# Kernel optimization log

Hardware: AMD Instinct MI355X
Metric: run time of the kernel (lower is better)

The kernel has to match this reference:

```python
import jax, jax.numpy as jnp
import numpy as np

B_CHUNK = 5          # hardcoded self.B in the module
GAMMA = 0.9865
BATCH, SEQ, FEAT, DIM = 8, 4000, 256, 256


def setup_inputs() -> dict:
    key = jax.random.key(0)
    ks = jax.random.split(key, 6)
    xq = jax.random.normal(ks[0], (BATCH, SEQ, FEAT), jnp.float32)
    xk = jax.random.normal(ks[1], (BATCH, SEQ, FEAT), jnp.float32)
    xv = jax.random.normal(ks[2], (BATCH, SEQ, FEAT), jnp.float32)
    scale = 1.0 / np.sqrt(FEAT).astype(np.float32)
    Wq = jax.random.normal(ks[3], (FEAT, DIM), jnp.float32) * scale
    Wk = jax.random.normal(ks[4], (FEAT, DIM), jnp.float32) * scale
    Wv = jax.random.normal(ks[5], (FEAT, DIM), jnp.float32) * scale
    return {"xq": xq, "xk": xk, "xv": xv, "Wq": Wq, "Wk": Wk, "Wv": Wv}


def reference(xq, xk, xv, Wq, Wk, Wv):
    gamma = jnp.float32(GAMMA)
    B = B_CHUNK
    b, seq, _ = xq.shape
    dim = Wq.shape[1]
    n = seq // B  # number of chunks

    # projections, chunked: [b, n, B, dim]
    Q = (xq @ Wq).reshape(b, n, B, dim)
    K = (xk @ Wk).reshape(b, n, B, dim)
    V = (xv @ Wv).reshape(b, n, B, dim)

    chunk_idx = jnp.arange(n, dtype=jnp.float32)
    # Z[i] = gamma^(B - i - 1) (per-chunk scalar, as in original)
    Z = gamma ** (jnp.float32(B) - chunk_idx - 1.0)
    Vz = V * Z[None, :, None, None]

    # intra-chunk decay matrix: L[i,j] = gamma^(j-i) for i >= j, else 0
    pos = jnp.arange(B, dtype=jnp.float32)
    L = jnp.tril(gamma ** (pos[None, :] - pos[:, None]))

    # intra-chunk term: (Q K^T * L) @ V, vectorized over all chunks
    S = jnp.einsum('bnid,bnjd->bnij', Q, K)          # [b, n, B, B]
    intra = jnp.einsum('bnij,bnjd->bnid', S * L, V)  # [b, n, B, dim]

    # cross-chunk recurrence: R[i] = K_i^T Vz_i + gamma^B R[i-1]
    # X[i-1] += Q_i @ R[i-1] * gamma^(i+1)
    Qn = jnp.moveaxis(Q, 1, 0)   # [n, b, B, dim]
    Kn = jnp.moveaxis(K, 1, 0)
    Vzn = jnp.moveaxis(Vz, 1, 0)
    gB = gamma ** B

    def step(R_prev, inp):
        qi, ki, vzi, i = inp
        cross_prev = jnp.einsum('bod,bde->boe', qi, R_prev) * gamma ** (i + 1.0)
        R_new = jnp.einsum('bod,boe->bde', ki, vzi) + gB * R_prev
        return R_new, cross_prev

    R0 = jnp.zeros((b, dim, dim), xq.dtype)
    _, ys = jax.lax.scan(step, R0, (Qn, Kn, Vzn, chunk_idx))  # ys[i] = cross for chunk i-1
    cross = jnp.concatenate([ys[1:], jnp.zeros_like(ys[:1])], axis=0)  # last chunk has no cross term
    cross = jnp.moveaxis(cross, 0, 1)  # [b, n, B, dim]

    X = intra + cross
    return X.reshape(b, seq, dim)
```

## Files before the change

### kernel.cpp

```cpp
#include <hip/hip_runtime.h>
#include <cmath>

#define GAMMA 0.9865f
#define L2G   -0.01960905f
#define BATCH 8
#define SEQ   4000
#define CSUP  25
#define GSUP  32
#define RPG   125

typedef _Float16 half8 __attribute__((ext_vector_type(8)));
typedef _Float16 half4 __attribute__((ext_vector_type(4)));
typedef float    floatx4 __attribute__((ext_vector_type(4)));

__device__ __forceinline__ float gpow(float e) { return exp2f(e * L2G); }

__global__ __launch_bounds__(256) void wt_convert(
    const float* __restrict__ Wq, const float* __restrict__ Wk, const float* __restrict__ Wv,
    _Float16* __restrict__ Wt) {
    int t = blockIdx.x * 256 + threadIdx.x;
    int mat = t >> 16, rem = t & 65535;
    int n = rem >> 8, k = rem & 255;
    const float* W = (mat == 0) ? Wq : (mat == 1) ? Wk : Wv;
    Wt[(size_t)mat * 65536 + n * 256 + k] = (_Float16)W[k * 256 + n];
}

__global__ __launch_bounds__(256, 2) void qkv_gemm_f16(
    const float* __restrict__ xq, const float* __restrict__ xk, const float* __restrict__ xv,
    const _Float16* __restrict__ WtAll,
    _Float16* __restrict__ Qb, _Float16* __restrict__ Kb, _Float16* __restrict__ Vb) {
    int op = blockIdx.y;
    const float* x = (op == 0) ? xq : (op == 1) ? xk : xv;
    const _Float16* Wt = WtAll + (size_t)op * 65536;
    _Float16* dst = (op == 0) ? Qb : (op == 1) ? Kb : Vb;

    __shared__ _Float16 Xs[128][40];
    __shared__ _Float16 WsT[256][40];

    int t = threadIdx.x;
    int lane = t & 63, wave = t >> 6;
    int ln = lane & 15, q8 = (lane >> 4) << 3, q4 = (lane >> 4) << 2;
    int row0 = blockIdx.x * 128;

    floatx4 acc[8][4] = {};

    for (int dt = 0; dt < 8; ++dt) {
        int k0 = dt * 32;
#pragma unroll
        for (int i = 0; i < 4; ++i) {
            int idx = t + i * 256;
            int m = idx >> 3, kk = (idx & 7) << 2;
            floatx4 v = *(const floatx4*)&x[(size_t)(row0 + m) * 256 + k0 + kk];
            half4 h; h[0] = (_Float16)v[0]; h[1] = (_Float16)v[1];
            h[2] = (_Float16)v[2]; h[3] = (_Float16)v[3];
            *(half4*)&Xs[m][kk] = h;
        }
#pragma unroll
        for (int i = 0; i < 4; ++i) {
            int idx = t + i * 256;
            int n = idx >> 2, kk = (idx & 3) << 3;
            *(half8*)&WsT[n][kk] = *(const half8*)&Wt[n * 256 + k0 + kk];
        }
        __syncthreads();
        half8 af[8];
#pragma unroll
        for (int mi = 0; mi < 8; ++mi) af[mi] = *(const half8*)&Xs[mi * 16 + ln][q8];
#pragma unroll
        for (int ni = 0; ni < 4; ++ni) {
            half8 bf = *(const half8*)&WsT[(wave * 4 + ni) * 16 + ln][q8];
#pragma unroll
            for (int mi = 0; mi < 8; ++mi)
                acc[mi][ni] = __builtin_amdgcn_mfma_f32_16x16x32_f16(af[mi], bf, acc[mi][ni], 0, 0, 0);
        }
        __syncthreads();
    }
#pragma unroll
    for (int mi = 0; mi < 8; ++mi)
#pragma unroll
        for (int ni = 0; ni < 4; ++ni)
#pragma unroll
            for (int r = 0; r < 4; ++r) {
                int row = row0 + mi * 16 + q4 + r;
                int col = (wave * 4 + ni) * 16 + ln;
                dst[(size_t)row * 256 + col] = (_Float16)acc[mi][ni][r];
            }
}

__global__ __launch_bounds__(256, 2) void chunk_states_mfma(
    const _Float16* __restrict__ Kb, const _Float16* __restrict__ Vb,
    _Float16* __restrict__ Wh) {
    int eh = blockIdx.x, g = blockIdx.y, b = blockIdx.z;
    int t = threadIdx.x, lane = t & 63, wave = t >> 6;
    int ln = lane & 15, q8 = (lane >> 4) << 3, q4 = (lane >> 4) << 2;
    __shared__ _Float16 Vs[32 * 137];
    __shared__ _Float16 Ks[32 * 265];
    size_t base_row = (size_t)b * SEQ + g * RPG;
    floatx4 acc[8][4] = {};
    for (int kt = 0; kt < 4; ++kt) {
        int r0 = kt * 32;
#pragma unroll
        for (int i = 0; i < 2; ++i) {
            int idx = t + i * 256;
            int r = idx >> 4, e8 = (idx & 15) << 3;
            half8 v = {};
            if (r0 + r < RPG) {
                v = *(const half8*)&Vb[(base_row + r0 + r) * 256 + eh * 128 + e8];
                int mloc = (r0 + r) / 5;
                float a = gpow((float)(149 - 6 * mloc));
#pragma unroll
                for (int z = 0; z < 8; ++z) v[z] = (_Float16)((float)v[z] * a);
            }
#pragma unroll
            for (int z = 0; z < 8; ++z) Vs[r * 137 + e8 + z] = v[z];
        }
#pragma unroll
        for (int i = 0; i < 4; ++i) {
            int idx = t + i * 256;
            int r = idx >> 5, d8 = (idx & 31) << 3;
            half8 v = {};
            if (r0 + r < RPG) v = *(const half8*)&Kb[(base_row + r0 + r) * 256 + d8];
#pragma unroll
            for (int z = 0; z < 8; ++z) Ks[r * 265 + d8 + z] = v[z];
        }
        __syncthreads();
        half8 Af[8], Bf[4];
#pragma unroll
        for (int mi = 0; mi < 8; ++mi)
#pragma unroll
            for (int j = 0; j < 8; ++j) Af[mi][j] = Vs[(q8 + j) * 137 + mi * 16 + ln];
#pragma unroll
        for (int ni = 0; ni < 4; ++ni)
#pragma unroll
            for (int j = 0; j < 8; ++j) Bf[ni][j] = Ks[(q8 + j) * 265 + wave * 64 + ni * 16 + ln];
#pragma unroll
        for (int mi = 0; mi < 8; ++mi)
#pragma unroll
            for (int ni = 0; ni < 4; ++ni)
                acc[mi][ni] = __builtin_amdgcn_mfma_f32_16x16x32_f16(Af[mi], Bf[ni], acc[mi][ni], 0, 0, 0);
        __syncthreads();
    }
    size_t ob = ((size_t)(g * 8 + b)) << 16;
#pragma unroll
    for (int mi = 0; mi < 8; ++mi)
#pragma unroll
        for (int ni = 0; ni < 4; ++ni)
#pragma unroll
            for (int r = 0; r < 4; ++r) {
                int e = eh * 128 + mi * 16 + q4 + r;
                int d = wave * 64 + ni * 16 + ln;
                Wh[ob + (size_t)e * 256 + d] = (_Float16)acc[mi][ni][r];
            }
}

__global__ __launch_bounds__(256) void state_scan(
    const _Float16* __restrict__ Wh, _Float16* __restrict__ SprevT) {
    int t = blockIdx.x * 256 + threadIdx.x;
    int b = t >> 14;
    int idx = (t & 16383) << 2;
    const float gF = gpow(150.0f);
    float s[4] = {};
    for (int g = 0; g < GSUP; ++g) {
        size_t o = (((size_t)(g * 8 + b)) << 16) + idx;
        half4 w = *(const half4*)&Wh[o];
        half4 sv;
#pragma unroll
        for (int z = 0; z < 4; ++z) { sv[z] = (_Float16)s[z]; s[z] = (float)w[z] + gF * s[z]; }
        *(half4*)&SprevT[o] = sv;
    }
}

__global__ __launch_bounds__(256) void intra_sc(
    const _Float16* __restrict__ Qb, const _Float16* __restrict__ Kb, float* __restrict__ scw) {
    int b = blockIdx.y;
    int j = blockIdx.x * 4 + (threadIdx.x >> 6);
    int lane = threadIdx.x & 63;
    size_t base = ((size_t)b * SEQ + j * 5) * 256 + lane * 4;
    half4 qv[5], kv[5];
#pragma unroll
    for (int p = 0; p < 5; ++p) {
        qv[p] = *(const half4*)&Qb[base + p * 256];
        kv[p] = *(const half4*)&Kb[base + p * 256];
    }
#pragma unroll
    for (int p = 0; p < 5; ++p)
#pragma unroll
        for (int q = 0; q <= p; ++q) {
            float s = 0.f;
#pragma unroll
            for (int z = 0; z < 4; ++z) s += (float)qv[p][z] * (float)kv[q][z];
#pragma unroll
            for (int off = 32; off; off >>= 1) s += __shfl_xor(s, off, 64);
            if (lane == 0) scw[((size_t)b * 800 + j) * 25 + p * 5 + q] = s * gpow((float)(q - p));
        }
}

__global__ __launch_bounds__(256, 3) void cross_f16(
    const _Float16* __restrict__ Qb, const _Float16* __restrict__ Kb,
    const _Float16* __restrict__ Vb, const _Float16* __restrict__ SprevT,
    const float* __restrict__ scw, float* __restrict__ out) {
    int eq = blockIdx.x, g = blockIdx.y, b = blockIdx.z;
    int e0 = eq * 64;
    int t = threadIdx.x;
    int lane = t & 63, wave = t >> 6;
    int ln = lane & 15, q8 = (lane >> 4) << 3, q4 = (lane >> 4) << 2;
    int m4 = (wave >> 1) * 4;
    int c4 = (wave & 1) * 4;
    int e2 = (wave & 1) * 2;

    __shared__ float rtab[25];
    __shared__ float gtabm[25];
    __shared__ _Float16 PsB[128 * 130];
    __shared__ _Float16 VsB[64 * 130];

    if (t < 25) { rtab[t] = gpow((float)(6 * t + 7)); gtabm[t] = gpow((float)(6 * (t + 1))); }

    size_t kvbase = (size_t)b * SEQ + g * RPG;
    size_t sb = ((size_t)(g * 8 + b)) << 16;
    size_t qrow0 = (size_t)b * SEQ;

#pragma unroll
    for (int i = 0; i < 4; ++i) {
        int idx = t + i * 256;
        int cp = idx >> 3, e8 = (idx & 7) << 3;
        half8 v = {};
        if (cp < 125) v = *(const half8*)&Vb[(kvbase + cp) * 256 + e0 + e8];
#pragma unroll
        for (int z = 0; z < 8; ++z) VsB[(e8 + z) * 130 + cp] = v[z];
    }

    floatx4 pacc[4][4] = {};
    floatx4 acc[4][2] = {};

    for (int dt = 0; dt < 8; ++dt) {
        int d0 = dt * 32;
        half8 af[4];
#pragma unroll
        for (int mi = 0; mi < 4; ++mi) {
            int rp = (m4 + mi) * 16 + ln;
            int qr = g * RPG + 5 + rp;
            half8 v = {};
            if (rp < 125 && qr < SEQ) v = *(const half8*)&Qb[(qrow0 + qr) * 256 + d0 + q8];
            af[mi] = v;
        }
#pragma unroll
        for (int ci = 0; ci < 4; ++ci) {
            int cp = (c4 + ci) * 16 + ln;
            half8 bf = {};
            if (cp < 125) bf = *(const half8*)&Kb[(kvbase + cp) * 256 + d0 + q8];
#pragma unroll
            for (int mi = 0; mi < 4; ++mi)
                pacc[mi][ci] = __builtin_amdgcn_mfma_f32_16x16x32_f16(af[mi], bf, pacc[mi][ci], 0, 0, 0);
        }
#pragma unroll
        for (int ei = 0; ei < 2; ++ei) {
            half8 bf = *(const half8*)&SprevT[sb + (size_t)(e0 + (e2 + ei) * 16 + ln) * 256 + d0 + q8];
#pragma unroll
            for (int mi = 0; mi < 4; ++mi)
                acc[mi][ei] = __builtin_amdgcn_mfma_f32_16x16x32_f16(af[mi], bf, acc[mi][ei], 0, 0, 0);
        }
    }

    __syncthreads();

#pragma unroll
    for (int mi = 0; mi < 4; ++mi)
#pragma unroll
        for (int r = 0; r < 4; ++r) {
            int rp = (m4 + mi) * 16 + q4 + r;
            int rc = rp / 5;
            float rs = 0.f;
            if (rp < 125 && !(g == GSUP - 1 && rc == CSUP - 1)) rs = rtab[rc];
            acc[mi][0][r] *= rs;
            acc[mi][1][r] *= rs;
        }

#pragma unroll
    for (int mi = 0; mi < 4; ++mi)
#pragma unroll
        for (int ci = 0; ci < 4; ++ci)
#pragma unroll
            for (int r = 0; r < 4; ++r) {
                int rp = (m4 + mi) * 16 + q4 + r;
                int cp = (c4 + ci) * 16 + ln;
                int rc = rp / 5, cc = cp / 5;
                float w = 0.f;
                if (rp < 125 && cp < 125 && cc <= rc && !(g == GSUP - 1 && rc == CSUP - 1))
                    w = gtabm[rc - cc];
                PsB[rp * 130 + cp] = (_Float16)(pacc[mi][ci][r] * w);
            }
    __syncthreads();

#pragma unroll
    for (int ct = 0; ct < 4; ++ct) {
        int cp0 = ct * 32;
        half8 paf[4];
#pragma unroll
        for (int mi = 0; mi < 4; ++mi)
#pragma unroll
            for (int j = 0; j < 8; ++j)
                paf[mi][j] = PsB[((m4 + mi) * 16 + ln) * 130 + cp0 + q8 + j];
#pragma unroll
        for (int ei = 0; ei < 2; ++ei) {
            half8 bv;
#pragma unroll
            for (int j = 0; j < 8; ++j)
                bv[j] = VsB[((e2 + ei) * 16 + ln) * 130 + cp0 + q8 + j];
#pragma unroll
            for (int mi = 0; mi < 4; ++mi)
                acc[mi][ei] = __builtin_amdgcn_mfma_f32_16x16x32_f16(paf[mi], bv, acc[mi][ei], 0, 0, 0);
        }
    }

#pragma unroll
    for (int mi = 0; mi < 4; ++mi)
#pragma unroll
        for (int r = 0; r < 4; ++r) {
            int rp = (m4 + mi) * 16 + q4 + r;
            if (rp < 125) {
                int rc = rp / 5, pp = rp - rc * 5;
                const float* srow = scw + ((size_t)b * 800 + g * 25 + rc) * 25 + pp * 5;
                float a0 = acc[mi][0][r], a1 = acc[mi][1][r];
                for (int q = 0; q <= pp; ++q) {
                    float s = srow[q];
                    a0 += s * (float)VsB[(e2 * 16 + ln) * 130 + rc * 5 + q];
                    a1 += s * (float)VsB[((e2 + 1) * 16 + ln) * 130 + rc * 5 + q];
                }
                size_t orow = ((size_t)b * SEQ + g * RPG + rp) * 256;
                out[orow + e0 + e2 * 16 + ln] = a0;
                out[orow + e0 + (e2 + 1) * 16 + ln] = a1;
            }
        }
}

extern "C" void kernel_launch(void* const* d_in, const int* in_sizes, int n_in,
                              void* d_out, int out_size, void* d_ws, size_t ws_size,
                              hipStream_t stream) {
    const float* xq = (const float*)d_in[0];
    const float* xk = (const float*)d_in[1];
    const float* xv = (const float*)d_in[2];
    const float* Wq = (const float*)d_in[3];
    const float* Wk = (const float*)d_in[4];
    const float* Wv = (const float*)d_in[5];
    float* out = (float*)d_out;

    const size_t NELEM = (size_t)SEQ * BATCH * 256;
    _Float16* Qb = (_Float16*)d_ws;
    _Float16* Kb = Qb + NELEM;
    _Float16* Vb = Kb + NELEM;
    _Float16* Wt = Vb + NELEM;
    _Float16* Wh = Wt + 196608;
    _Float16* SprevT = Wh + (size_t)GSUP * BATCH * 65536;
    float* scw = (float*)(SprevT + (size_t)GSUP * BATCH * 65536);

    wt_convert<<<dim3(768), 256, 0, stream>>>(Wq, Wk, Wv, Wt);
    qkv_gemm_f16<<<dim3(250, 3), 256, 0, stream>>>(xq, xk, xv, Wt, Qb, Kb, Vb);
    chunk_states_mfma<<<dim3(2, 32, 8), 256, 0, stream>>>(Kb, Vb, Wh);
    state_scan<<<dim3(512), 256, 0, stream>>>(Wh, SprevT);
    intra_sc<<<dim3(200, 8), 256, 0, stream>>>(Qb, Kb, scw);
    cross_f16<<<dim3(4, 32, 8), 256, 0, stream>>>(Qb, Kb, Vb, SprevT, scw, out);
}
```

Baseline: 290.5 us.

## Retile cross kernel by row halves with LDS-staged double-buffered Q/K and tiled state

The cross kernel now tiles over two 64-row halves with all 256 output columns per block, instead of four 64-column slabs. This removes the redundant recomputation of the QK^T score block across column slabs. Q and K tiles are staged through double-buffered LDS with prefetch. The state-scan writes the prefix states in an MFMA-fragment-tiled layout so the B operands load contiguously, and V is transposed into LDS in two halves that reuse the staging memory. The trade-off is half as many blocks (less parallelism), higher accumulator register pressure, and more LDS per block.

```diff
diff --git a/kernel.cpp b/kernel.cpp
--- a/kernel.cpp
+++ b/kernel.cpp
@@ -153,19 +153,23 @@
 }
 
 __global__ __launch_bounds__(256) void state_scan(
-    const _Float16* __restrict__ Wh, _Float16* __restrict__ SprevT) {
+    const _Float16* __restrict__ Wh, _Float16* __restrict__ Sx) {
     int t = blockIdx.x * 256 + threadIdx.x;
     int b = t >> 14;
-    int idx = (t & 16383) << 2;
+    int r = t & 16383;
+    int e = r >> 6;
+    int dc = (r & 63) << 2;
+    int T = (dc >> 5) * 16 + (e >> 4);
+    int off = T * 512 + (e & 15) * 32 + (dc & 31);
     const float gF = gpow(150.0f);
     float s[4] = {};
     for (int g = 0; g < GSUP; ++g) {
-        size_t o = (((size_t)(g * 8 + b)) << 16) + idx;
-        half4 w = *(const half4*)&Wh[o];
+        size_t ibase = ((size_t)(g * 8 + b)) << 16;
+        half4 w = *(const half4*)&Wh[ibase + e * 256 + dc];
         half4 sv;
 #pragma unroll
         for (int z = 0; z < 4; ++z) { sv[z] = (_Float16)s[z]; s[z] = (float)w[z] + gF * s[z]; }
-        *(half4*)&SprevT[o] = sv;
+        *(half4*)&Sx[ibase + off] = sv;
     }
 }
 
@@ -196,140 +200,168 @@
 
 __global__ __launch_bounds__(256, 3) void cross_f16(
     const _Float16* __restrict__ Qb, const _Float16* __restrict__ Kb,
-    const _Float16* __restrict__ Vb, const _Float16* __restrict__ SprevT,
+    const _Float16* __restrict__ Vb, const _Float16* __restrict__ Sx,
     const float* __restrict__ scw, float* __restrict__ out) {
-    int eq = blockIdx.x, g = blockIdx.y, b = blockIdx.z;
-    int e0 = eq * 64;
+    int rh = blockIdx.x, g = blockIdx.y, b = blockIdx.z;
     int t = threadIdx.x;
-    int lane = t & 63, wave = t >> 6;
-    int ln = lane & 15, q8 = (lane >> 4) << 3, q4 = (lane >> 4) << 2;
-    int m4 = (wave >> 1) * 4;
-    int c4 = (wave & 1) * 4;
-    int e2 = (wave & 1) * 2;
-
-    __shared__ float rtab[25];
-    __shared__ float gtabm[25];
-    __shared__ _Float16 PsB[128 * 130];
-    __shared__ _Float16 VsB[64 * 130];
+    int lane = t & 63, eq = t >> 6;
+    int ln = lane & 15, qd = lane >> 4;
+    int q8 = qd << 3, q4 = qd << 2;
+
+    __shared__ __align__(16) char smem[52432];
+    _Float16* stage = (_Float16*)smem;
+    _Float16* PsB = (_Float16*)(smem + 34816);
+    float* rtab = (float*)(smem + 52224);
+    float* gtabm = rtab + 25;
 
     if (t < 25) { rtab[t] = gpow((float)(6 * t + 7)); gtabm[t] = gpow((float)(6 * (t + 1))); }
 
     size_t kvbase = (size_t)b * SEQ + g * RPG;
-    size_t sb = ((size_t)(g * 8 + b)) << 16;
-    size_t qrow0 = (size_t)b * SEQ;
-
-#pragma unroll
-    for (int i = 0; i < 4; ++i) {
-        int idx = t + i * 256;
-        int cp = idx >> 3, e8 = (idx & 7) << 3;
-        half8 v = {};
-        if (cp < 125) v = *(const half8*)&Vb[(kvbase + cp) * 256 + e0 + e8];
-#pragma unroll
-        for (int z = 0; z < 8; ++z) VsB[(e8 + z) * 130 + cp] = v[z];
-    }
-
-    floatx4 pacc[4][4] = {};
-    floatx4 acc[4][2] = {};
-
+    size_t sxb = ((size_t)(g * 8 + b)) << 16;
+    size_t qtop = (size_t)b * SEQ;
+
+    int sm = t >> 2;
+    int skk = (t & 3) << 3;
+    int rpgQ = rh * 64 + sm;
+    int qr = g * RPG + 5 + rpgQ;
+    bool qok = (rpgQ < RPG) && (qr < SEQ);
+    int cpb = sm + 64;
+
+    floatx4 pacc[4][2] = {};
+    floatx4 acc[4][4] = {};
+
+    {
+        half8 pq = {}, pk0, pk1 = {};
+        if (qok) pq = *(const half8*)&Qb[(qtop + qr) * 256 + skk];
+        pk0 = *(const half8*)&Kb[(kvbase + sm) * 256 + skk];
+        if (cpb < RPG) pk1 = *(const half8*)&Kb[(kvbase + cpb) * 256 + skk];
+        *(half8*)&stage[sm * 40 + skk] = pq;
+        *(half8*)&stage[2560 + sm * 40 + skk] = pk0;
+        *(half8*)&stage[2560 + cpb * 40 + skk] = pk1;
+    }
+    __syncthreads();
+
+#pragma unroll
     for (int dt = 0; dt < 8; ++dt) {
-        int d0 = dt * 32;
+        const _Float16* Qc = stage + (dt & 1) * 7680;
+        const _Float16* Kc = Qc + 2560;
+        half8 pq = {}, pk0 = {}, pk1 = {};
+        if (dt < 7) {
+            int d0n = (dt + 1) * 32;
+            if (qok) pq = *(const half8*)&Qb[(qtop + qr) * 256 + d0n + skk];
+            pk0 = *(const half8*)&Kb[(kvbase + sm) * 256 + d0n + skk];
+            if (cpb < RPG) pk1 = *(const half8*)&Kb[(kvbase + cpb) * 256 + d0n + skk];
+        }
+        half8 sf[4];
+#pragma unroll
+        for (int ei = 0; ei < 4; ++ei) {
+            int Et = (ei >> 1) * 8 + eq * 2 + (ei & 1);
+            sf[ei] = *(const half8*)&Sx[sxb + (size_t)(dt * 16 + Et) * 512 + ln * 32 + q8];
+        }
         half8 af[4];
 #pragma unroll
-        for (int mi = 0; mi < 4; ++mi) {
-            int rp = (m4 + mi) * 16 + ln;
-            int qr = g * RPG + 5 + rp;
+        for (int mi = 0; mi < 4; ++mi) af[mi] = *(const half8*)&Qc[(mi * 16 + ln) * 40 + q8];
+#pragma unroll
+        for (int ci = 0; ci < 2; ++ci) {
+            half8 bk = *(const half8*)&Kc[(eq * 32 + ci * 16 + ln) * 40 + q8];
+#pragma unroll
+            for (int mi = 0; mi < 4; ++mi)
+                pacc[mi][ci] = __builtin_amdgcn_mfma_f32_16x16x32_f16(af[mi], bk, pacc[mi][ci], 0, 0, 0);
+        }
+#pragma unroll
+        for (int ei = 0; ei < 4; ++ei)
+#pragma unroll
+            for (int mi = 0; mi < 4; ++mi)
+                acc[mi][ei] = __builtin_amdgcn_mfma_f32_16x16x32_f16(af[mi], sf[ei], acc[mi][ei], 0, 0, 0);
+        if (dt < 7) {
+            _Float16* Qn = stage + ((dt + 1) & 1) * 7680;
+            *(half8*)&Qn[sm * 40 + skk] = pq;
+            *(half8*)&Qn[2560 + sm * 40 + skk] = pk0;
+            *(half8*)&Qn[2560 + cpb * 40 + skk] = pk1;
+        }
+        __syncthreads();
+    }
+
+#pragma unroll
+    for (int mi = 0; mi < 4; ++mi)
+#pragma unroll
+        for (int r = 0; r < 4; ++r) {
+            int rpg = rh * 64 + mi * 16 + q4 + r;
+            float rs = 0.f;
+            if (rpg < RPG) {
+                int rc = rpg / 5;
+                if (!(g == GSUP - 1 && rc == CSUP - 1)) rs = rtab[rc];
+            }
+#pragma unroll
+            for (int ei = 0; ei < 4; ++ei) acc[mi][ei][r] *= rs;
+        }
+
+#pragma unroll
+    for (int mi = 0; mi < 4; ++mi)
+#pragma unroll
+        for (int ci = 0; ci < 2; ++ci)
+#pragma unroll
+            for (int r = 0; r < 4; ++r) {
+                int rpl = mi * 16 + q4 + r;
+                int rpg = rh * 64 + rpl;
+                int cp = eq * 32 + ci * 16 + ln;
+                float w = 0.f;
+                if (rpg < RPG && cp < RPG) {
+                    int rc = rpg / 5, cc = cp / 5;
+                    if (cc <= rc && !(g == GSUP - 1 && rc == CSUP - 1)) w = gtabm[rc - cc];
+                }
+                PsB[rpl * 136 + cp] = (_Float16)(pacc[mi][ci][r] * w);
+            }
+
+    _Float16* VsT = (_Float16*)smem;
+
+#pragma unroll
+    for (int h = 0; h < 2; ++h) {
+        if (h == 1) __syncthreads();
+#pragma unroll
+        for (int i = 0; i < 8; ++i) {
+            int idx = t + i * 256;
+            int cp = idx & 127;
+            int eb = idx >> 7;
             half8 v = {};
-            if (rp < 125 && qr < SEQ) v = *(const half8*)&Qb[(qrow0 + qr) * 256 + d0 + q8];
-            af[mi] = v;
-        }
-#pragma unroll
-        for (int ci = 0; ci < 4; ++ci) {
-            int cp = (c4 + ci) * 16 + ln;
-            half8 bf = {};
-            if (cp < 125) bf = *(const half8*)&Kb[(kvbase + cp) * 256 + d0 + q8];
+            if (cp < RPG) v = *(const half8*)&Vb[(kvbase + cp) * 256 + h * 128 + eb * 8];
+#pragma unroll
+            for (int z = 0; z < 8; ++z) VsT[(eb * 8 + z) * 136 + cp] = v[z];
+        }
+        __syncthreads();
+#pragma unroll
+        for (int ct = 0; ct < 4; ++ct) {
+            half8 ap[4];
 #pragma unroll
             for (int mi = 0; mi < 4; ++mi)
-                pacc[mi][ci] = __builtin_amdgcn_mfma_f32_16x16x32_f16(af[mi], bf, pacc[mi][ci], 0, 0, 0);
-        }
-#pragma unroll
-        for (int ei = 0; ei < 2; ++ei) {
-            half8 bf = *(const half8*)&SprevT[sb + (size_t)(e0 + (e2 + ei) * 16 + ln) * 256 + d0 + q8];
-#pragma unroll
-            for (int mi = 0; mi < 4; ++mi)
-                acc[mi][ei] = __builtin_amdgcn_mfma_f32_16x16x32_f16(af[mi], bf, acc[mi][ei], 0, 0, 0);
-        }
-    }
-
-    __syncthreads();
-
-#pragma unroll
-    for (int mi = 0; mi < 4; ++mi)
-#pragma unroll
-        for (int r = 0; r < 4; ++r) {
-            int rp = (m4 + mi) * 16 + q4 + r;
-            int rc = rp / 5;
-            float rs = 0.f;
-            if (rp < 125 && !(g == GSUP - 1 && rc == CSUP - 1)) rs = rtab[rc];
-            acc[mi][0][r] *= rs;
-            acc[mi][1][r] *= rs;
-        }
-
-#pragma unroll
-    for (int mi = 0; mi < 4; ++mi)
-#pragma unroll
-        for (int ci = 0; ci < 4; ++ci)
+                ap[mi] = *(const half8*)&PsB[(mi * 16 + ln) * 136 + ct * 32 + q8];
+#pragma unroll
+            for (int j = 0; j < 2; ++j) {
+                half8 bv = *(const half8*)&VsT[(eq * 32 + j * 16 + ln) * 136 + ct * 32 + q8];
+#pragma unroll
+                for (int mi = 0; mi < 4; ++mi)
+                    acc[mi][h * 2 + j] = __builtin_amdgcn_mfma_f32_16x16x32_f16(ap[mi], bv, acc[mi][h * 2 + j], 0, 0, 0);
+            }
+        }
+#pragma unroll
+        for (int mi = 0; mi < 4; ++mi)
 #pragma unroll
             for (int r = 0; r < 4; ++r) {
-                int rp = (m4 + mi) * 16 + q4 + r;
-                int cp = (c4 + ci) * 16 + ln;
-                int rc = rp / 5, cc = cp / 5;
-                float w = 0.f;
-                if (rp < 125 && cp < 125 && cc <= rc && !(g == GSUP - 1 && rc == CSUP - 1))
-                    w = gtabm[rc - cc];
-                PsB[rp * 130 + cp] = (_Float16)(pacc[mi][ci][r] * w);
-            }
-    __syncthreads();
-
-#pragma unroll
-    for (int ct = 0; ct < 4; ++ct) {
-        int cp0 = ct * 32;
-        half8 paf[4];
-#pragma unroll
-        for (int mi = 0; mi < 4; ++mi)
-#pragma unroll
-            for (int j = 0; j < 8; ++j)
-                paf[mi][j] = PsB[((m4 + mi) * 16 + ln) * 130 + cp0 + q8 + j];
-#pragma unroll
-        for (int ei = 0; ei < 2; ++ei) {
-            half8 bv;
-#pragma unroll
-            for (int j = 0; j < 8; ++j)
-                bv[j] = VsB[((e2 + ei) * 16 + ln) * 130 + cp0 + q8 + j];
-#pragma unroll
-            for (int mi = 0; mi < 4; ++mi)
-                acc[mi][ei] = __builtin_amdgcn_mfma_f32_16x16x32_f16(paf[mi], bv, acc[mi][ei], 0, 0, 0);
-        }
-    }
-
-#pragma unroll
-    for (int mi = 0; mi < 4; ++mi)
-#pragma unroll
-        for (int r = 0; r < 4; ++r) {
-            int rp = (m4 + mi) * 16 + q4 + r;
-            if (rp < 125) {
-                int rc = rp / 5, pp = rp - rc * 5;
-                const float* srow = scw + ((size_t)b * 800 + g * 25 + rc) * 25 + pp * 5;
-                float a0 = acc[mi][0][r], a1 = acc[mi][1][r];
-                for (int q = 0; q <= pp; ++q) {
-                    float s = srow[q];
-                    a0 += s * (float)VsB[(e2 * 16 + ln) * 130 + rc * 5 + q];
-                    a1 += s * (float)VsB[((e2 + 1) * 16 + ln) * 130 + rc * 5 + q];
+                int rpg = rh * 64 + mi * 16 + q4 + r;
+                if (rpg < RPG) {
+                    int rc = rpg / 5, pp = rpg - rc * 5;
+                    const float* srow = scw + ((size_t)b * 800 + g * 25 + rc) * 25 + pp * 5;
+#pragma unroll
+                    for (int j = 0; j < 2; ++j) {
+                        int el = eq * 32 + j * 16 + ln;
+                        float a = acc[mi][h * 2 + j][r];
+                        for (int q = 0; q <= pp; ++q)
+                            a += srow[q] * (float)VsT[el * 136 + rc * 5 + q];
+                        out[((size_t)b * SEQ + g * RPG + rpg) * 256 + h * 128 + el] = a;
+                    }
                 }
-                size_t orow = ((size_t)b * SEQ + g * RPG + rp) * 256;
-                out[orow + e0 + e2 * 16 + ln] = a0;
-                out[orow + e0 + (e2 + 1) * 16 + ln] = a1;
-            }
-        }
+            }
+    }
 }
 
 extern "C" void kernel_launch(void* const* d_in, const int* in_sizes, int n_in,
@@ -349,13 +381,13 @@
     _Float16* Vb = Kb + NELEM;
     _Float16* Wt = Vb + NELEM;
     _Float16* Wh = Wt + 196608;
-    _Float16* SprevT = Wh + (size_t)GSUP * BATCH * 65536;
-    float* scw = (float*)(SprevT + (size_t)GSUP * BATCH * 65536);
+    _Float16* Sx = Wh + (size_t)GSUP * BATCH * 65536;
+    float* scw = (float*)(Sx + (size_t)GSUP * BATCH * 65536);
 
     wt_convert<<<dim3(768), 256, 0, stream>>>(Wq, Wk, Wv, Wt);
     qkv_gemm_f16<<<dim3(250, 3), 256, 0, stream>>>(xq, xk, xv, Wt, Qb, Kb, Vb);
     chunk_states_mfma<<<dim3(2, 32, 8), 256, 0, stream>>>(Kb, Vb, Wh);
-    state_scan<<<dim3(512), 256, 0, stream>>>(Wh, SprevT);
+    state_scan<<<dim3(512), 256, 0, stream>>>(Wh, Sx);
     intra_sc<<<dim3(200, 8), 256, 0, stream>>>(Qb, Kb, scw);
-    cross_f16<<<dim3(4, 32, 8), 256, 0, stream>>>(Qb, Kb, Vb, SprevT, scw, out);
-}
+    cross_f16<<<dim3(2, 32, 8), 256, 0, stream>>>(Qb, Kb, Vb, Sx, scw, out);
+}
```

Measured after the change: 277.5 us. 4.5% less time.
